# Kernel tuning notes

Hardware: AMD Instinct MI355X
Metric: run time of the kernel (lower is better)

The kernel has to match this reference:

```python
import jax, jax.numpy as jnp
import numpy as np
from math import ceil

H, W = 360, 640
H_, W_ = ceil(H / 32) * 32, ceil(W / 32) * 32  # 384, 640
SF = 2
TIMES = [k / SF for k in range(1, SF)]  # [0.5]


def conv(x, w, b=None, pad=1):
    y = jax.lax.conv_general_dilated(x, w, (1, 1), [(pad, pad), (pad, pad)],
                                     dimension_numbers=('NCHW', 'OIHW', 'NCHW'))
    if b is not None:
        y = y + b[None, :, None, None]
    return y


def resize_ac(x, Hn, Wn):
    # bilinear, align_corners=True, NCHW
    B, C, Hs, Ws = x.shape
    if (Hn, Wn) == (Hs, Ws):
        return x
    ys = jnp.linspace(0.0, Hs - 1.0, Hn, dtype=x.dtype)
    xs = jnp.linspace(0.0, Ws - 1.0, Wn, dtype=x.dtype)
    y0 = jnp.floor(ys).astype(jnp.int32); y1 = jnp.minimum(y0 + 1, Hs - 1)
    x0 = jnp.floor(xs).astype(jnp.int32); x1 = jnp.minimum(x0 + 1, Ws - 1)
    wy = (ys - y0)[None, None, :, None]
    wx = (xs - x0)[None, None, None, :]
    rows = x[:, :, y0, :] * (1 - wy) + x[:, :, y1, :] * wy      # [B,C,Hn,Ws]
    return rows[:, :, :, x0] * (1 - wx) + rows[:, :, :, x1] * wx  # [B,C,Hn,Wn]


def warp(img, flow):
    # backward warp with bilinear sampling, zeros padding (grid_sample semantics)
    B, C, Hs, Ws = img.shape
    gy, gx = jnp.meshgrid(jnp.arange(Hs, dtype=img.dtype), jnp.arange(Ws, dtype=img.dtype), indexing='ij')
    xq = gx[None] + flow[:, 0]  # [B,H,W]
    yq = gy[None] + flow[:, 1]

    def samp(im, xx, yy):  # im [C,H,W]
        x0 = jnp.floor(xx).astype(jnp.int32); x1 = x0 + 1
        y0 = jnp.floor(yy).astype(jnp.int32); y1 = y0 + 1
        wx = xx - x0; wy = yy - y0

        def g(xi, yi):
            valid = ((xi >= 0) & (xi < Ws) & (yi >= 0) & (yi < Hs)).astype(im.dtype)
            xc = jnp.clip(xi, 0, Ws - 1); yc = jnp.clip(yi, 0, Hs - 1)
            return im[:, yc, xc] * valid[None]  # [C,H,W] gather

        return (g(x0, y0) * (1 - wx) * (1 - wy) + g(x1, y0) * wx * (1 - wy)
                + g(x0, y1) * (1 - wx) * wy + g(x1, y1) * wx * wy)

    return jax.vmap(samp)(img, xq, yq)


def bmnet(x6, t, w1, b1, w2, b2):
    # stand-in bilateral motion net: conv stack conditioned on time channel -> 2-ch flow
    tch = jnp.full_like(x6[:, :1], t)
    h = jax.nn.relu(conv(jnp.concatenate([x6, tch], 1), w1, b1, 1))
    return conv(h, w2, b2, 1)


def local_expand(x):
    # [B,C,H,W] -> [B,C*9,H,W] of 3x3 neighborhoods (c-major, kernel-position minor)
    B, C, Hs, Ws = x.shape
    xp = jnp.pad(x, ((0, 0), (0, 0), (1, 1), (1, 1)))
    pats = [xp[:, :, dy:dy + Hs, dx:dx + Ws] for dy in range(3) for dx in range(3)]
    return jnp.stack(pats, 2).reshape(B, C * 9, Hs, Ws)


def dynfilter(cand, DF):
    # cand [B,6,H,W], DF [B,54,H,W] -> [B,1,H,W] spatially-varying weighted gather
    pe = local_expand(cand)
    return jnp.einsum('bkhw,bkhw->bhw', pe, DF)[:, None]


def reference(I0, I1, target, ctx_W, bm_W1, bm_b1, bm_W2, bm_b2, df_W1, df_b1, df_W2, df_b2, count):
    tgt = target.at[count].set(I0[0])
    c = count + 1
    pair_r = resize_ac(jnp.concatenate([I0, I1], 1), H_, W_)
    scl = jnp.array([W / W_, H / H_], jnp.float32).reshape(1, 2, 1, 1)
    F01 = resize_ac(bmnet(pair_r, 0.0, bm_W1, bm_b1, bm_W2, bm_b2) * 2.0, H, W) * scl
    F10 = resize_ac(bmnet(pair_r, 1.0, bm_W1, bm_b1, bm_W2, bm_b2) * -2.0, H, W) * scl
    CI0 = jax.nn.relu(conv(I0, ctx_W, None, 3))
    CI1 = jax.nn.relu(conv(I1, ctx_W, None, 3))
    X0 = jnp.concatenate([I0, CI0], 1)  # [1,67,H,W]
    X1 = jnp.concatenate([I1, CI1], 1)
    for t in TIMES:
        ti = 1.0 - t
        BM = resize_ac(bmnet(pair_r, t, bm_W1, bm_b1, bm_W2, bm_b2), H, W) * scl
        C1 = warp(X0, -t * F01)
        C2 = warp(X1, ti * F01)
        C3 = warp(X0, t * F10)
        C4 = warp(X1, (t - 1.0) * F10)
        C5 = warp(X0, BM * (-2.0 * t))
        C6 = warp(X1, BM * (2.0 * ti))
        inp = jnp.concatenate([I0, C1, C2, C3, C4, C5, C6, I1], 1)  # [1,408,H,W]
        h = jax.nn.relu(conv(inp, df_W1, df_b1, 1))
        DF = jax.nn.softmax(conv(h, df_W2, df_b2, 1), axis=1)  # [1,54,H,W]
        cand = inp[:, 3:-3]  # [1,402,H,W]
        R = dynfilter(cand[:, 0::67], DF)
        G = dynfilter(cand[:, 1::67], DF)
        Bc = dynfilter(cand[:, 2::67], DF)
        tgt = tgt.at[c, 0].set(R[0, 0]).at[c, 1].set(G[0, 0]).at[c, 2].set(Bc[0, 0])
        c += 1
    return tgt, c


def setup_inputs() -> dict:
    key = jax.random.key(0)
    ks = jax.random.split(key, 8)
    he = lambda k, shp: jax.random.normal(k, shp, jnp.float32) * np.float32((2.0 / (shp[1] * shp[2] * shp[3])) ** 0.5)
    return {
        'I0': jax.random.uniform(ks[0], (1, 3, H, W), jnp.float32),
        'I1': jax.random.uniform(ks[1], (1, 3, H, W), jnp.float32),
        'target': jnp.zeros((3, 3, H, W), jnp.float32),
        'ctx_W': he(ks[2], (64, 3, 7, 7)),
        'bm_W1': he(ks[3], (32, 7, 3, 3)),
        'bm_b1': jnp.zeros((32,), jnp.float32),
        'bm_W2': he(ks[4], (2, 32, 3, 3)) * np.float32(0.1),  # small flows
        'bm_b2': jnp.zeros((2,), jnp.float32),
        'df_W1': he(ks[5], (32, 408, 3, 3)),
        'df_b1': jnp.zeros((32,), jnp.float32),
        'df_W2': he(ks[6], (54, 32, 3, 3)),
        'df_b2': jnp.zeros((54,), jnp.float32),
        'count': 0,
    }
```

## Files before the change

kernel.cpp:

```cpp
#include <hip/hip_runtime.h>
#include <hip/hip_bf16.h>
#include <hip/hip_fp16.h>

#define Hh 360
#define Ww 640
#define HW (Hh*Ww)
#define Hr 384
#define HWr (Hr*Ww)

#define TW 48
#define TH 4
#define WCOLS 50
#define SROWS 6
#define NXT 14
#define NYT 90
#define NBLK (NXT*NYT)

#define WTW 16
#define WTH 8
#define WCL 18
#define WSR 10
#define WCCH 72
#define WNXT 40
#define WNYT 45
#define WNBLK (WNXT*WNYT)

#define CRS 24

typedef __hip_bfloat16 bf16;
typedef __attribute__((ext_vector_type(8))) short short8v;
typedef __attribute__((ext_vector_type(4))) short short4v;
typedef __attribute__((ext_vector_type(4))) float f32x4;
typedef __attribute__((ext_vector_type(2))) float f32x2;
typedef __attribute__((ext_vector_type(4))) int i32x4;

static __device__ __forceinline__ bf16 f2b(float v) { return __float2bfloat16(v); }
static __device__ __forceinline__ short f2bs(float v) { bf16 t = __float2bfloat16(v); return *(short*)&t; }
static __device__ __forceinline__ float bs2f(short s) {
    unsigned u = ((unsigned)(unsigned short)s) << 16;
    float f; __builtin_memcpy(&f, &u, 4); return f;
}

#if defined(__has_builtin)
#if __has_builtin(__builtin_amdgcn_cvt_pk_f32_fp8) && __has_builtin(__builtin_amdgcn_cvt_pk_fp8_f32)
#define FP8_HW 1
#endif
#endif

static __device__ __forceinline__ void fp8dec4(int dw, float* f) {
#ifdef FP8_HW
    f32x2 lo = __builtin_amdgcn_cvt_pk_f32_fp8(dw, false);
    f32x2 hi = __builtin_amdgcn_cvt_pk_f32_fp8(dw, true);
    f[0] = lo[0]; f[1] = lo[1]; f[2] = hi[0]; f[3] = hi[1];
#else
    #pragma unroll
    for (int k = 0; k < 4; k++) {
        int u = (dw >> (8 * k)) & 0xFF;
        int e = (u >> 3) & 15, m = u & 7;
        int mant = e ? ((8 + m) << (e - 1)) : m;
        float v = (float)mant * 0x1p-9f;
        f[k] = (u & 0x80) ? -v : v;
    }
#endif
}

static __device__ __forceinline__ int fp8enc4(float a, float b, float c, float d) {
#ifdef FP8_HW
    int r = __builtin_amdgcn_cvt_pk_fp8_f32(a, b, 0, false);
    r = __builtin_amdgcn_cvt_pk_fp8_f32(c, d, r, true);
    return r;
#else
    float vals[4] = {a, b, c, d};
    int r = 0;
    #pragma unroll
    for (int k = 0; k < 4; k++) {
        float v = vals[k];
        unsigned bits; __builtin_memcpy(&bits, &v, 4);
        unsigned s = bits >> 31;
        float av = fabsf(v);
        int u;
        if (!(av >= 0x1p-10f)) u = 0;
        else if (av >= 448.0f) u = 0x7E;
        else {
            int e; float fr = frexpf(av, &e);
            (void)fr;
            int E = e + 6;
            if (E < 1) {
                u = (int)roundf(av * 512.0f);
            } else {
                float sc = exp2f((float)(10 - E));
                int mm = (int)roundf(av * sc) - 8;
                if (mm == 8) { mm = 0; E++; }
                u = (E > 15) ? 0x7E : ((E << 3) | mm);
            }
        }
        r |= ((u | (s << 7)) & 0xFF) << (8 * k);
    }
    return r;
#endif
}

__global__ void front_all(const float* __restrict__ I0, const float* __restrict__ I1,
                          const float* __restrict__ target, const int* __restrict__ count,
                          const float* __restrict__ dfW1, const float* __restrict__ dfW2,
                          const float* __restrict__ ctxW, const float* __restrict__ bmW2,
                          const float* __restrict__ bmW1,
                          float* __restrict__ out, bf16* __restrict__ I4,
                          bf16* __restrict__ pr8,
                          bf16* __restrict__ wfrag, bf16* __restrict__ wfrag2,
                          bf16* __restrict__ wctx, float* __restrict__ w2t,
                          bf16* __restrict__ wbm1, float* __restrict__ tsW) {
    int idx = blockIdx.x * 256 + threadIdx.x;
    if (idx < 6 * HW + 1) {
        if (idx < 3 * HW) {
            out[idx] = I0[idx];
        } else if (idx < 6 * HW) {
            size_t off = (size_t)6 * HW + (idx - 3 * HW);
            out[off] = target[off];
        } else {
            out[(size_t)9 * HW] = (float)(count[0] + 2);
        }
        return;
    }
    idx -= 6 * HW + 1;
    if (idx < 2 * HW) {
        int z = idx / HW, p = idx % HW;
        const float* img = z ? I1 : I0;
        short4v v;
        v[0] = f2bs(img[p]);
        v[1] = f2bs(img[(size_t)HW + p]);
        v[2] = f2bs(img[(size_t)2 * HW + p]);
        v[3] = 0;
        *(short4v*)((short*)I4 + (size_t)idx * 4) = v;
        return;
    }
    idx -= 2 * HW;
    if (idx < HWr) {
        int p = idx;
        int x = p % Ww, y = p / Ww;
        float ys = y * (359.0f / 383.0f);
        int y0 = (int)floorf(ys);
        if (y0 > 359) y0 = 359;
        int y1 = y0 + 1; if (y1 > 359) y1 = 359;
        float wy = ys - (float)y0;
        short8v v;
        #pragma unroll
        for (int c = 0; c < 6; c++) {
            const float* src = (c < 3) ? (I0 + (size_t)c * HW) : (I1 + (size_t)(c - 3) * HW);
            v[c] = f2bs(src[y0 * Ww + x] * (1.0f - wy) + src[y1 * Ww + x] * wy);
        }
        v[6] = 0; v[7] = 0;
        *(short8v*)((short*)pr8 + (size_t)p * 8) = v;
        return;
    }
    idx -= HWr;
    if (idx < 165888) {
        int j = idx & 7;
        int t = idx >> 3;
        int l = t & 63; t >>= 6;
        int m = t & 1; t >>= 1;
        int chunk = t % 3; t /= 3;
        int q = t % 9;
        int w = t / 9;
        int oc = m * 16 + (l & 15);
        int ch = chunk * 32 + ((l >> 4) << 3) + j;
        int ic = -1;
        if (ch < 67) ic = 3 + 67 * w + ch;
        else if (ch < 70) {
            if (w == 0) ic = ch - 67;
            else if (w == 5) ic = 405 + (ch - 67);
        }
        float v = (ic >= 0) ? dfW1[((oc * 408 + ic) * 3 + q / 3) * 3 + (q % 3)] : 0.0f;
        wfrag[idx] = f2b(v);
        return;
    }
    idx -= 165888;
    if (idx < 18432) {
        int j = idx & 7;
        int t = idx >> 3;
        int l = t & 63; t >>= 6;
        int n = t & 3; t >>= 2;
        int q = t;
        int oc = n * 16 + (l & 15);
        int kch = ((l >> 4) << 3) + j;
        float v = (oc < 54) ? dfW2[((oc * 32 + kch) * 3 + q / 3) * 3 + (q % 3)] : 0.0f;
        wfrag2[idx] = f2b(v);
        return;
    }
    idx -= 18432;
    if (idx < 14336) {
        int j = idx & 7;
        int t = idx >> 3;
        int l = t & 63; t >>= 6;
        int n = t & 3;
        int ky = t >> 2;
        int oc = n * 16 + (l & 15);
        int k = ((l >> 4) << 3) + j;
        int kx = k >> 2, ic = k & 3;
        float v = (kx < 7 && ic < 3) ? ctxW[oc * 147 + ic * 49 + ky * 7 + kx] : 0.0f;
        wctx[idx] = f2b(v);
        return;
    }
    idx -= 14336;
    if (idx < 576) {
        int o = idx & 1;
        int t = idx >> 1;
        int i = t % 32;
        int q = t / 32;
        w2t[idx] = bmW2[o * 288 + i * 9 + q];
        return;
    }
    idx -= 576;
    if (idx < 3072) {
        int j = idx & 7;
        int t = idx >> 3;
        int l = t & 63; t >>= 6;
        int m = t & 1;
        int ky = t >> 1;
        int oc = m * 16 + (l & 15);
        int k = ((l >> 4) << 3) + j;
        int kx = k >> 3, ic = k & 7;
        float v = (kx < 3 && ic < 6) ? bmW1[oc * 63 + ic * 9 + ky * 3 + kx] : 0.0f;
        wbm1[idx] = f2b(v);
        return;
    }
    idx -= 3072;
    if (idx < 288) {
        int o = idx & 31;
        int c = idx >> 5;
        int vy = c / 3, vx = c % 3;
        float s = 0.0f;
        for (int q = 0; q < 9; q++) {
            int ky = q / 3, kx = q % 3;
            bool okY = !((vy == 1 && ky == 0) || (vy == 2 && ky == 2));
            bool okX = !((vx == 1 && kx == 0) || (vx == 2 && kx == 2));
            if (okY && okX) s += bmW1[o * 63 + 54 + q];
        }
        tsW[idx] = s;
    }
}

__global__ __launch_bounds__(256, 4) void bm_base_mfma(const bf16* __restrict__ pr8,
                                                       const bf16* __restrict__ wbm1,
                                                       const float* __restrict__ b1,
                                                       const float* __restrict__ tsW,
                                                       bf16* __restrict__ h) {
    __shared__ short raw8[SROWS * WCOLS * 8];
    __shared__ short outb[192 * 32];
    __shared__ float tsl[288];
    const int tid = threadIdx.x;
    const int bx = blockIdx.x % NXT;
    const int by = blockIdx.x / NXT;
    const int x0 = bx * TW, y0 = by * TH;
    const short8v z8 = {0, 0, 0, 0, 0, 0, 0, 0};

    for (int e = tid; e < 288; e += 256) tsl[e] = tsW[e];
    for (int e = tid; e < SROWS * WCOLS; e += 256) {
        int c = e % WCOLS, r = e / WCOLS;
        int gy = y0 - 1 + r, gx = x0 - 1 + c;
        short8v v = z8;
        if (gy >= 0 && gy < Hr && gx >= 0 && gx < Ww)
            v = *(const short8v*)((const short*)pr8 + ((size_t)gy * Ww + gx) * 8);
        *(short8v*)(raw8 + e * 8) = v;
    }
    __syncthreads();

    const int wv = tid >> 6, lane = tid & 63, l15 = lane & 15, lg = lane >> 4;
    f32x4 acc[3][2];
    {
        float bv0 = b1[l15], bv1 = b1[16 + l15];
        #pragma unroll
        for (int pt = 0; pt < 3; pt++)
            #pragma unroll
            for (int r = 0; r < 4; r++) { acc[pt][0][r] = bv0; acc[pt][1][r] = bv1; }
    }
    #pragma unroll 1
    for (int ky = 0; ky < 3; ky++) {
        short8v bw0 = ((const short8v*)wbm1)[(ky * 2 + 0) * 64 + lane];
        short8v bw1 = ((const short8v*)wbm1)[(ky * 2 + 1) * 64 + lane];
        #pragma unroll
        for (int pt = 0; pt < 3; pt++) {
            int col = pt * 16 + l15;
            short8v a = z8;
            if (lg < 3) a = *(const short8v*)(raw8 + ((wv + ky) * WCOLS + col + lg) * 8);
            acc[pt][0] = __builtin_amdgcn_mfma_f32_16x16x32_bf16(a, bw0, acc[pt][0], 0, 0, 0);
            acc[pt][1] = __builtin_amdgcn_mfma_f32_16x16x32_bf16(a, bw1, acc[pt][1], 0, 0, 0);
        }
    }
    #pragma unroll
    for (int pt = 0; pt < 3; pt++)
        #pragma unroll
        for (int m = 0; m < 2; m++)
            #pragma unroll
            for (int r = 0; r < 4; r++) {
                int px = pt * 16 + (lg << 2) + r;
                outb[(wv * 48 + px) * 32 + m * 16 + l15] = f2bs(acc[pt][m][r]);
            }
    __syncthreads();
    #pragma unroll
    for (int it = 0; it < 3; it++) {
        int e = it * 256 + tid;
        int oc8 = e & 3;
        int px = (e >> 2) % 48;
        int rw = e / 192;
        int gx = x0 + px;
        if (gx < Ww) {
            int gy = y0 + rw;
            short8v bsev = *(const short8v*)(outb + (rw * 48 + px) * 32 + oc8 * 8);
            int vy = (gy == 0) ? 1 : ((gy == Hr - 1) ? 2 : 0);
            int vx = (gx == 0) ? 1 : ((gx == Ww - 1) ? 2 : 0);
            const float* tp = tsl + (vy * 3 + vx) * 32 + oc8 * 8;
            float bsef[8], tsf[8];
            #pragma unroll
            for (int j = 0; j < 8; j++) { bsef[j] = bs2f(bsev[j]); tsf[j] = tp[j]; }
            #pragma unroll
            for (int z = 0; z < 3; z++) {
                float tz = (z == 0) ? 0.0f : ((z == 1) ? 1.0f : 0.5f);
                short8v o;
                #pragma unroll
                for (int j = 0; j < 8; j++)
                    o[j] = f2bs(fmaxf(bsef[j] + tz * tsf[j], 0.0f));
                *(short8v*)((short*)h + ((size_t)z * HWr + (size_t)gy * Ww + gx) * 32 + oc8 * 8) = o;
            }
        }
    }
}

__global__ __launch_bounds__(256) void bm_conv2i(const bf16* __restrict__ h,
                                                 const float* __restrict__ w2t,
                                                 const float* __restrict__ b2,
                                                 float* __restrict__ bmout) {
    int p = blockIdx.x * 256 + threadIdx.x;
    if (p >= HWr) return;
    int z = blockIdx.y;
    int x = p % Ww, y = p / Ww;
    const short* hz = (const short*)h + (size_t)z * HWr * 32;
    float a0 = b2[0], a1 = b2[1];
    for (int ky = 0; ky < 3; ky++) {
        int ny = y + ky - 1;
        if (ny < 0 || ny >= Hr) continue;
        for (int kx = 0; kx < 3; kx++) {
            int nx = x + kx - 1;
            if (nx < 0 || nx >= Ww) continue;
            const float* wp = w2t + (ky * 3 + kx) * 64;
            const short* ip = hz + ((size_t)ny * Ww + nx) * 32;
            #pragma unroll
            for (int ck = 0; ck < 4; ck++) {
                short8v v = *(const short8v*)(ip + ck * 8);
                #pragma unroll
                for (int j = 0; j < 8; j++) {
                    float f = bs2f(v[j]);
                    a0 = fmaf(f, wp[(ck * 8 + j) * 2 + 0], a0);
                    a1 = fmaf(f, wp[(ck * 8 + j) * 2 + 1], a1);
                }
            }
        }
    }
    float f = (z == 0) ? 2.0f : ((z == 1) ? -2.0f : 1.0f);
    bmout[(size_t)(z * 2 + 0) * HWr + p] = a0 * f;
    bmout[(size_t)(z * 2 + 1) * HWr + p] = a1 * f;
}

__global__ __launch_bounds__(256) void flow_resize(const float* __restrict__ bmout,
                                                   float* __restrict__ flows) {
    int p = blockIdx.x * 256 + threadIdx.x;
    if (p >= HW) return;
    int x = p % Ww;
    int y = p / Ww;
    float ys = y * (383.0f / 359.0f);
    int y0 = (int)floorf(ys);
    if (y0 > 383) y0 = 383;
    int y1 = y0 + 1; if (y1 > 383) y1 = 383;
    float wy = ys - (float)y0;
    float o[6];
    #pragma unroll
    for (int zc = 0; zc < 6; zc++) {
        const float* src = bmout + (size_t)zc * HWr;
        float v = src[y0 * Ww + x] * (1.0f - wy) + src[y1 * Ww + x] * wy;
        o[zc] = v * ((zc & 1) ? (360.0f / 384.0f) : 1.0f);
    }
    #pragma unroll
    for (int zc = 0; zc < 6; zc++)
        flows[(size_t)p * 6 + zc] = o[zc];
}

__global__ __launch_bounds__(256, 2) void ctx_mfma(const bf16* __restrict__ I4,
                                                   const bf16* __restrict__ wctx,
                                                   bf16* __restrict__ Xrgb,
                                                   unsigned char* __restrict__ Xq) {
    __shared__ short raw4[10 * 54 * 4];
    __shared__ short outb[192 * 72];
    const int tid = threadIdx.x;
    const int z = blockIdx.y;
    const int bx = blockIdx.x % NXT;
    const int by = blockIdx.x / NXT;
    const int x0 = bx * TW, y0 = by * TH;
    const short* img4 = (const short*)I4 + (size_t)z * HW * 4;
    const short4v z4 = {0, 0, 0, 0};

    for (int e = tid; e < 540; e += 256) {
        int c = e % 54, r = e / 54;
        int gy = y0 - 3 + r, gx = x0 - 3 + c;
        short4v v = z4;
        if (gy >= 0 && gy < Hh && gx >= 0 && gx < Ww)
            v = *(const short4v*)(img4 + ((size_t)gy * Ww + gx) * 4);
        *(short4v*)(raw4 + e * 4) = v;
    }
    __syncthreads();

    const int wv = tid >> 6, lane = tid & 63, l15 = lane & 15, lg = lane >> 4;
    f32x4 acc[3][4];
    #pragma unroll
    for (int pt = 0; pt < 3; pt++)
        #pragma unroll
        for (int n = 0; n < 4; n++)
            #pragma unroll
            for (int r = 0; r < 4; r++) acc[pt][n][r] = 0.0f;

    #pragma unroll 1
    for (int ky = 0; ky < 7; ky++) {
        short8v bw[4];
        #pragma unroll
        for (int n = 0; n < 4; n++)
            bw[n] = ((const short8v*)wctx)[(ky * 4 + n) * 64 + lane];
        #pragma unroll
        for (int pt = 0; pt < 3; pt++) {
            int col = pt * 16 + l15;
            int base = ((wv + ky) * 54 + col + 2 * lg) * 4;
            short4v lo = *(const short4v*)(raw4 + base);
            short4v hi = (lg == 3) ? z4 : *(const short4v*)(raw4 + base + 4);
            short8v a = __builtin_shufflevector(lo, hi, 0, 1, 2, 3, 4, 5, 6, 7);
            #pragma unroll
            for (int n = 0; n < 4; n++)
                acc[pt][n] = __builtin_amdgcn_mfma_f32_16x16x32_bf16(a, bw[n], acc[pt][n], 0, 0, 0);
        }
    }

    for (int e = tid; e < 576; e += 256) {
        int ic = e % 3, p = e / 3;
        outb[p * 72 + ic] = raw4[((p / 48 + 3) * 54 + (p % 48) + 3) * 4 + ic];
    }
    for (int e = tid; e < 960; e += 256) {
        int c = e % 5, p = e / 5;
        outb[p * 72 + 67 + c] = 0;
    }
    #pragma unroll
    for (int pt = 0; pt < 3; pt++)
        #pragma unroll
        for (int n = 0; n < 4; n++)
            #pragma unroll
            for (int r = 0; r < 4; r++) {
                int px = pt * 16 + (lg << 2) + r;
                outb[(wv * 48 + px) * 72 + 3 + n * 16 + l15] = f2bs(fmaxf(acc[pt][n][r], 0.0f));
            }
    __syncthreads();
    for (int e = tid; e < 960; e += 256) {
        int part = e % 5, p = e / 5;
        int gx = x0 + p % 48, gy = y0 + p / 48;
        if (gx >= Ww) continue;
        size_t pix = (size_t)z * HW + (size_t)gy * Ww + gx;
        if (part == 0) {
            *(short8v*)((short*)Xrgb + pix * 8) = *(const short8v*)(outb + p * 72);
        } else {
            const short* src = outb + p * 72 + 8 + (part - 1) * 16;
            i32x4 r;
            #pragma unroll
            for (int d = 0; d < 4; d++)
                r[d] = fp8enc4(bs2f(src[4 * d + 0]), bs2f(src[4 * d + 1]),
                               bs2f(src[4 * d + 2]), bs2f(src[4 * d + 3]));
            *(i32x4*)(Xq + pix * 64 + (size_t)(part - 1) * 16) = r;
        }
    }
}

__global__ __launch_bounds__(256, 3) void wdf_all(const bf16* __restrict__ Xrgb,
                                                  const unsigned char* __restrict__ Xq,
                                                  const float* __restrict__ flows,
                                                  const bf16* __restrict__ wfrag,
                                                  const float* __restrict__ b1,
                                                  const float* __restrict__ I0,
                                                  const float* __restrict__ I1,
                                                  bf16* __restrict__ hdf,
                                                  bf16* __restrict__ candRGB) {
    __shared__ short ldsA[WSR * WCL * WCCH];
    __shared__ short ldsB[WSR * WCL * WCCH];
    const int tid = threadIdx.x;
    const int bid = blockIdx.x;
    const int wg = (bid & 7) * (WNBLK / 8) + (bid >> 3);
    const int bx = wg % WNXT;
    const int by = wg / WNXT;
    const int x0 = bx * WTW, y0 = by * WTH;
    const short8v z8 = {0, 0, 0, 0, 0, 0, 0, 0};

    const int wv = tid >> 6;
    const int lane = tid & 63;
    const int l15 = lane & 15;
    const int lg = lane >> 4;

    auto stage = [&](int w, short* dstb) {
        const int fz = (w < 2) ? 0 : ((w < 4) ? 1 : 2);
        const float fac = ((w < 4) ? 0.5f : 1.0f) *
                          ((w == 1 || w == 2 || w == 5) ? 1.0f : -1.0f);
        const short* xrgb = (const short*)Xrgb + (size_t)(w & 1) * HW * 8;
        const unsigned char* xq = Xq + (size_t)(w & 1) * HW * 64;
        const float* img = (w == 0) ? I0 : I1;
        int e = tid;
        if (e < WSR * WCL) {
            int c = e % WCL, r = e / WCL;
            int gy = y0 - 1 + r, gx = x0 - 1 + c;
            short* dst = dstb + e * WCCH;
            if (gy < 0 || gy >= Hh || gx < 0 || gx >= Ww) {
                #pragma unroll
                for (int ck = 0; ck < 9; ck++) *(short8v*)(dst + ck * 8) = z8;
            } else {
                int p = gy * Ww + gx;
                float2 fl = *(const float2*)(flows + (size_t)p * 6 + fz * 2);
                float xqf = (float)gx + fl.x * fac;
                float yqf = (float)gy + fl.y * fac;
                float fx0 = floorf(xqf), fy0 = floorf(yqf);
                int sx0 = (int)fx0, sy0 = (int)fy0;
                int sx1 = sx0 + 1, sy1 = sy0 + 1;
                float wx = xqf - fx0, wy = yqf - fy0;
                float vx0 = (sx0 >= 0 && sx0 < Ww) ? 1.0f : 0.0f;
                float vx1 = (sx1 >= 0 && sx1 < Ww) ? 1.0f : 0.0f;
                float vy0 = (sy0 >= 0 && sy0 < Hh) ? 1.0f : 0.0f;
                float vy1 = (sy1 >= 0 && sy1 < Hh) ? 1.0f : 0.0f;
                int cx0 = min(max(sx0, 0), Ww - 1), cx1 = min(max(sx1, 0), Ww - 1);
                int cy0 = min(max(sy0, 0), Hh - 1), cy1 = min(max(sy1, 0), Hh - 1);
                float w00 = (1.0f - wx) * (1.0f - wy) * vx0 * vy0;
                float w10 = wx * (1.0f - wy) * vx1 * vy0;
                float w01 = (1.0f - wx) * wy * vx0 * vy1;
                float w11 = wx * wy * vx1 * vy1;
                size_t i00 = (size_t)cy0 * Ww + cx0;
                size_t i10 = (size_t)cy0 * Ww + cx1;
                size_t i01 = (size_t)cy1 * Ww + cx0;
                size_t i11 = (size_t)cy1 * Ww + cx1;
                short8v g00 = *(const short8v*)(xrgb + i00 * 8);
                short8v g10 = *(const short8v*)(xrgb + i10 * 8);
                short8v g01 = *(const short8v*)(xrgb + i01 * 8);
                short8v g11 = *(const short8v*)(xrgb + i11 * 8);
                const i32x4* q00 = (const i32x4*)(xq + i00 * 64);
                const i32x4* q10 = (const i32x4*)(xq + i10 * 64);
                const i32x4* q01 = (const i32x4*)(xq + i01 * 64);
                const i32x4* q11 = (const i32x4*)(xq + i11 * 64);
                i32x4 qa[4], qb[4], qc[4], qd[4];
                #pragma unroll
                for (int c2 = 0; c2 < 4; c2++) {
                    qa[c2] = q00[c2]; qb[c2] = q10[c2];
                    qc[c2] = q01[c2]; qd[c2] = q11[c2];
                }
                short rgb0, rgb1, rgb2;
                {
                    short8v o;
                    #pragma unroll
                    for (int j = 0; j < 8; j++) {
                        float v = w00 * bs2f(g00[j]) + w10 * bs2f(g10[j]) +
                                  w01 * bs2f(g01[j]) + w11 * bs2f(g11[j]);
                        o[j] = f2bs(v);
                    }
                    rgb0 = o[0]; rgb1 = o[1]; rgb2 = o[2];
                    *(short8v*)(dst) = o;
                }
                #pragma unroll
                for (int c2 = 0; c2 < 4; c2++) {
                    short o16[16];
                    #pragma unroll
                    for (int d = 0; d < 4; d++) {
                        float fa[4], fb[4], fc[4], fd[4];
                        fp8dec4(qa[c2][d], fa);
                        fp8dec4(qb[c2][d], fb);
                        fp8dec4(qc[c2][d], fc);
                        fp8dec4(qd[c2][d], fd);
                        #pragma unroll
                        for (int j = 0; j < 4; j++) {
                            float v = w00 * fa[j] + w10 * fb[j] +
                                      w01 * fc[j] + w11 * fd[j];
                            o16[4 * d + j] = f2bs(v);
                        }
                    }
                    short8v o1, o2;
                    #pragma unroll
                    for (int j = 0; j < 8; j++) { o1[j] = o16[j]; o2[j] = o16[8 + j]; }
                    *(short8v*)(dst + 8 + c2 * 16) = o1;
                    *(short8v*)(dst + 8 + c2 * 16 + 8) = o2;
                }
                if (w == 0 || w == 5) {
                    dst[67] = f2bs(img[p]);
                    dst[68] = f2bs(img[(size_t)HW + p]);
                    dst[69] = f2bs(img[(size_t)2 * HW + p]);
                }
                if (r >= 1 && r <= WTH && c >= 1 && c <= WTW) {
                    short* crp = (short*)candRGB + (size_t)p * CRS + w * 3;
                    crp[0] = rgb0; crp[1] = rgb1; crp[2] = rgb2;
                }
            }
        }
    };

    f32x4 acc[2][2];
    {
        float bv0 = b1[l15], bv1 = b1[16 + l15];
        #pragma unroll
        for (int rt = 0; rt < 2; rt++)
            #pragma unroll
            for (int r = 0; r < 4; r++) { acc[rt][0][r] = bv0; acc[rt][1][r] = bv1; }
    }

    stage(0, ldsA);
    __syncthreads();

    #pragma unroll 1
    for (int wi = 0; wi < 6; wi++) {
        const int w = (wi < 3) ? (2 * wi) : (2 * (wi - 3) + 1);
        short* curb = (wi & 1) ? ldsB : ldsA;

        const short8v* wf = (const short8v*)(wfrag + (size_t)w * 9 * 3 * 2 * 64 * 8);
        __builtin_amdgcn_s_setprio(1);
        #pragma unroll 1
        for (int ky = 0; ky < 3; ky++) {
            #pragma unroll
            for (int kx = 0; kx < 3; kx++) {
                const int dx = kx - 1;
                const int q = ky * 3 + kx;
                #pragma unroll
                for (int chunk = 0; chunk < 3; chunk++) {
                    short8v bw0 = wf[((q * 3 + chunk) * 2 + 0) * 64 + lane];
                    short8v bw1 = wf[((q * 3 + chunk) * 2 + 1) * 64 + lane];
                    const int koff = (chunk < 2) ? (chunk * 32 + (lg << 3)) : 64;
                    #pragma unroll
                    for (int rt = 0; rt < 2; rt++) {
                        int srow = 2 * wv + rt + ky;
                        int col = 1 + dx + l15;
                        const short8v* apt = (const short8v*)(curb + (srow * WCL + col) * WCCH + koff);
                        short8v a = *apt;
                        acc[rt][0] = __builtin_amdgcn_mfma_f32_16x16x32_bf16(a, bw0, acc[rt][0], 0, 0, 0);
                        acc[rt][1] = __builtin_amdgcn_mfma_f32_16x16x32_bf16(a, bw1, acc[rt][1], 0, 0, 0);
                    }
                }
            }
        }
        __builtin_amdgcn_s_setprio(0);

        if (wi < 5) {
            const int wn = ((wi + 1) < 3) ? (2 * (wi + 1)) : (2 * (wi + 1 - 3) + 1);
            stage(wn, (wi & 1) ? ldsA : ldsB);
        }
        __syncthreads();
    }

    #pragma unroll
    for (int rt = 0; rt < 2; rt++) {
        #pragma unroll
        for (int m = 0; m < 2; m++) {
            #pragma unroll
            for (int r = 0; r < 4; r++) {
                float v = fmaxf(acc[rt][m][r], 0.0f);
                int pxx = (lg << 2) + r;
                ldsA[((2 * wv + rt) * 16 + pxx) * 32 + m * 16 + l15] = f2bs(v);
            }
        }
    }
    __syncthreads();
    #pragma unroll
    for (int it = 0; it < 2; it++) {
        int e = it * 256 + tid;
        int oc8 = e & 3;
        int px = e >> 2;
        int row = px >> 4, xl = px & 15;
        short8v v = *(const short8v*)(ldsA + px * 32 + oc8 * 8);
        *(short8v*)((short*)hdf + ((size_t)(y0 + row) * Ww + x0 + xl) * 32 + oc8 * 8) = v;
    }
}

__global__ __launch_bounds__(256, 3) void df2_mfma(const bf16* __restrict__ hdf,
                                                   const bf16* __restrict__ wf2,
                                                   const float* __restrict__ b2,
                                                   const bf16* __restrict__ candRGB,
                                                   float* __restrict__ out) {
    __shared__ float smem[192 * 65];
    short* sst = (short*)smem;
    const int tid = threadIdx.x;
    const int bx = blockIdx.x % NXT;
    const int by = blockIdx.x / NXT;
    const int x0 = bx * TW, y0 = by * TH;

    const short* hs = (const short*)hdf;
    for (int e = tid; e < SROWS * WCOLS * 4; e += 256) {
        int v = e & 3;
        int c = (e >> 2) % WCOLS;
        int r = e / (4 * WCOLS);
        int gy = y0 - 1 + r, gx = x0 - 1 + c;
        short8v val = {0, 0, 0, 0, 0, 0, 0, 0};
        if (gy >= 0 && gy < Hh && gx >= 0 && gx < Ww)
            val = *(const short8v*)(hs + ((size_t)gy * Ww + gx) * 32 + v * 8);
        *(short8v*)(sst + (r * WCOLS + c) * 32 + v * 8) = val;
    }
    __syncthreads();

    const int wv = tid >> 6, lane = tid & 63, l15 = lane & 15, lg = lane >> 4;
    f32x4 acc[3][4];
    #pragma unroll
    for (int n = 0; n < 4; n++) {
        int oc = n * 16 + l15;
        float bv = (oc < 54) ? b2[oc] : 0.0f;
        #pragma unroll
        for (int pt = 0; pt < 3; pt++)
            #pragma unroll
            for (int r = 0; r < 4; r++) acc[pt][n][r] = bv;
    }
    #pragma unroll 1
    for (int ky = 0; ky < 3; ky++) {
        int srow = wv + ky;
        #pragma unroll
        for (int kx = 0; kx < 3; kx++) {
            int dx = kx - 1, q = ky * 3 + kx;
            short8v bw[4];
            #pragma unroll
            for (int n = 0; n < 4; n++) bw[n] = ((const short8v*)wf2)[(q * 4 + n) * 64 + lane];
            #pragma unroll
            for (int pt = 0; pt < 3; pt++) {
                int col = 1 + pt * 16 + dx + l15;
                short8v a = *(const short8v*)(sst + (srow * WCOLS + col) * 32 + lg * 8);
                #pragma unroll
                for (int n = 0; n < 4; n++)
                    acc[pt][n] = __builtin_amdgcn_mfma_f32_16x16x32_bf16(a, bw[n], acc[pt][n], 0, 0, 0);
            }
        }
    }
    __syncthreads();
    #pragma unroll
    for (int pt = 0; pt < 3; pt++)
        #pragma unroll
        for (int n = 0; n < 4; n++)
            #pragma unroll
            for (int r = 0; r < 4; r++) {
                int px = wv * 48 + pt * 16 + (lg << 2) + r;
                smem[px * 65 + n * 16 + l15] = acc[pt][n][r];
            }
    __syncthreads();

    if (tid < 192) {
        int xl = tid % 48, yl = tid / 48;
        int gx = x0 + xl, gy = y0 + yl;
        if (gx < Ww) {
            const float* lp = smem + tid * 65;
            float m = lp[0];
            #pragma unroll
            for (int o = 1; o < 54; o++) m = fmaxf(m, lp[o]);
            float e[54]; float s = 0.f;
            #pragma unroll
            for (int o = 0; o < 54; o++) { e[o] = __expf(lp[o] - m); s += e[o]; }
            float inv = 1.0f / s;
            float rr = 0, gg = 0, bb = 0;
            const short* cr = (const short*)candRGB;
            #pragma unroll
            for (int dy = 0; dy < 3; dy++) {
                int ny = gy + dy - 1;
                if (ny < 0 || ny >= Hh) continue;
                #pragma unroll
                for (int dx = 0; dx < 3; dx++) {
                    int nx = gx + dx - 1;
                    if (nx < 0 || nx >= Ww) continue;
                    const short* cp = cr + ((size_t)ny * Ww + nx) * CRS;
                    short8v v0 = *(const short8v*)(cp);
                    short8v v1 = *(const short8v*)(cp + 8);
                    short8v v2 = *(const short8v*)(cp + 16);
                    float ch[18];
                    #pragma unroll
                    for (int j = 0; j < 8; j++) { ch[j] = bs2f(v0[j]); ch[8 + j] = bs2f(v1[j]); }
                    ch[16] = bs2f(v2[0]);
                    ch[17] = bs2f(v2[1]);
                    #pragma unroll
                    for (int c6 = 0; c6 < 6; c6++) {
                        float df = e[c6 * 9 + dy * 3 + dx];
                        rr = fmaf(ch[c6 * 3 + 0], df, rr);
                        gg = fmaf(ch[c6 * 3 + 1], df, gg);
                        bb = fmaf(ch[c6 * 3 + 2], df, bb);
                    }
                }
            }
            size_t gp = (size_t)gy * Ww + gx;
            out[(size_t)3 * HW + gp] = rr * inv;
            out[(size_t)4 * HW + gp] = gg * inv;
            out[(size_t)5 * HW + gp] = bb * inv;
        }
    }
}

static inline int cdiv(int a, int b) { return (a + b - 1) / b; }

extern "C" void kernel_launch(void* const* d_in, const int* in_sizes, int n_in,
                              void* d_out, int out_size, void* d_ws, size_t ws_size,
                              hipStream_t stream) {
    const float* I0 = (const float*)d_in[0];
    const float* I1 = (const float*)d_in[1];
    const float* target = (const float*)d_in[2];
    const float* ctx_W = (const float*)d_in[3];
    const float* bm_W1 = (const float*)d_in[4];
    const float* bm_b1 = (const float*)d_in[5];
    const float* bm_W2 = (const float*)d_in[6];
    const float* bm_b2 = (const float*)d_in[7];
    const float* df_W1 = (const float*)d_in[8];
    const float* df_b1 = (const float*)d_in[9];
    const float* df_W2 = (const float*)d_in[10];
    const float* df_b2 = (const float*)d_in[11];
    const int* count = (const int*)d_in[12];
    float* out = (float*)d_out;

    char* ws = (char*)d_ws;
    size_t off = 0;
    auto alloc = [&](size_t bytes) -> char* {
        char* p = ws + off;
        off += (bytes + 255) & ~(size_t)255;
        return p;
    };
    char* xreg = alloc((size_t)3 * HWr * 32 * 2);
    float* flows = (float*)alloc((size_t)HW * 6 * 4);
    bf16* candRGB = (bf16*)alloc((size_t)HW * CRS * 2);
    bf16* hdf = (bf16*)alloc((size_t)HW * 32 * 2);
    bf16* I4 = (bf16*)alloc((size_t)2 * HW * 4 * 2);
    bf16* pr8 = (bf16*)alloc((size_t)HWr * 8 * 2);
    float* bmout = (float*)alloc((size_t)6 * HWr * 4);
    bf16* wfrag = (bf16*)alloc((size_t)165888 * 2);
    bf16* wfrag2 = (bf16*)alloc((size_t)18432 * 2);
    bf16* wctx = (bf16*)alloc((size_t)14336 * 2);
    float* w2t = (float*)alloc((size_t)576 * 4);
    bf16* wbm1 = (bf16*)alloc((size_t)3072 * 2);
    float* tsW = (float*)alloc((size_t)288 * 4);
    size_t need = off;
    if (ws_size < need) return;

    bf16* h_bm = (bf16*)xreg;
    bf16* Xrgb = (bf16*)xreg;
    unsigned char* Xq = (unsigned char*)(xreg + (size_t)2 * HW * 8 * 2);

    const int FRONT_TOTAL = (6 * HW + 1) + 2 * HW + HWr + 202592;
    front_all<<<cdiv(FRONT_TOTAL, 256), 256, 0, stream>>>(
        I0, I1, target, count, df_W1, df_W2, ctx_W, bm_W2, bm_W1,
        out, I4, pr8, wfrag, wfrag2, wctx, w2t, wbm1, tsW);

    bm_base_mfma<<<NXT * (Hr / TH), 256, 0, stream>>>(pr8, wbm1, bm_b1, tsW, h_bm);
    dim3 g1(cdiv(HWr, 256), 3);
    bm_conv2i<<<g1, 256, 0, stream>>>(h_bm, w2t, bm_b2, bmout);
    flow_resize<<<cdiv(HW, 256), 256, 0, stream>>>(bmout, flows);

    dim3 gc(NBLK, 2);
    ctx_mfma<<<gc, 256, 0, stream>>>(I4, wctx, Xrgb, Xq);

    wdf_all<<<WNBLK, 256, 0, stream>>>(Xrgb, Xq, flows, wfrag, df_b1, I0, I1, hdf, candRGB);

    df2_mfma<<<NBLK, 256, 0, stream>>>(hdf, wfrag2, df_b2, candRGB, out);
}
```

Baseline: 252.7 us.

## Rewrite bm conv2 as LDS-tiled bf16 MFMA kernel with padded weight fragments

Replaces the scalar per-pixel 32->2 channel 3x3 convolution with an MFMA kernel that stages a halo tile of the hidden activations in shared memory. Each wave then computes 16-pixel strips using 16x16x32 bf16 MFMA, with the output channels zero-padded from 2 to 16. The weight prep in the front kernel now emits bf16 MFMA fragments instead of transposed fp32 weights. The aim is to cut redundant global loads and scalar FMAs, at the cost of wasted MFMA lanes on padded channels. Separately, ctx_mfma's launch bound is raised to 4 blocks per CU, which may increase register pressure.

Result: faster. 242.8 us (-3.9%).

```diff
diff --git a/kernel.cpp b/kernel.cpp
--- a/kernel.cpp
+++ b/kernel.cpp
@@ -108,7 +108,7 @@
                           float* __restrict__ out, bf16* __restrict__ I4,
                           bf16* __restrict__ pr8,
                           bf16* __restrict__ wfrag, bf16* __restrict__ wfrag2,
-                          bf16* __restrict__ wctx, float* __restrict__ w2t,
+                          bf16* __restrict__ wctx, bf16* __restrict__ wbm2,
                           bf16* __restrict__ wbm1, float* __restrict__ tsW) {
     int idx = blockIdx.x * 256 + threadIdx.x;
     if (idx < 6 * HW + 1) {
@@ -202,15 +202,18 @@
         return;
     }
     idx -= 14336;
-    if (idx < 576) {
-        int o = idx & 1;
-        int t = idx >> 1;
-        int i = t % 32;
-        int q = t / 32;
-        w2t[idx] = bmW2[o * 288 + i * 9 + q];
+    if (idx < 4608) {
+        int j = idx & 7;
+        int t = idx >> 3;
+        int l = t & 63;
+        int q = t >> 6;
+        int oc = l & 15;
+        int kch = ((l >> 4) << 3) + j;
+        float v = (oc < 2) ? bmW2[oc * 288 + kch * 9 + q] : 0.0f;
+        wbm2[idx] = f2b(v);
         return;
     }
-    idx -= 576;
+    idx -= 4608;
     if (idx < 3072) {
         int j = idx & 7;
         int t = idx >> 3;
@@ -326,39 +329,67 @@
     }
 }
 
-__global__ __launch_bounds__(256) void bm_conv2i(const bf16* __restrict__ h,
-                                                 const float* __restrict__ w2t,
-                                                 const float* __restrict__ b2,
-                                                 float* __restrict__ bmout) {
-    int p = blockIdx.x * 256 + threadIdx.x;
-    if (p >= HWr) return;
-    int z = blockIdx.y;
-    int x = p % Ww, y = p / Ww;
+__global__ __launch_bounds__(256, 4) void bm2_mfma(const bf16* __restrict__ h,
+                                                   const bf16* __restrict__ wbm2,
+                                                   const float* __restrict__ b2,
+                                                   float* __restrict__ bmout) {
+    __shared__ short sst[SROWS * WCOLS * 32];
+    const int tid = threadIdx.x;
+    const int z = blockIdx.y;
+    const int bx = blockIdx.x % NXT;
+    const int by = blockIdx.x / NXT;
+    const int x0 = bx * TW, y0 = by * TH;
+    const short8v z8 = {0, 0, 0, 0, 0, 0, 0, 0};
+
     const short* hz = (const short*)h + (size_t)z * HWr * 32;
-    float a0 = b2[0], a1 = b2[1];
+    for (int e = tid; e < SROWS * WCOLS * 4; e += 256) {
+        int v = e & 3;
+        int c = (e >> 2) % WCOLS;
+        int r = e / (4 * WCOLS);
+        int gy = y0 - 1 + r, gx = x0 - 1 + c;
+        short8v val = z8;
+        if (gy >= 0 && gy < Hr && gx >= 0 && gx < Ww)
+            val = *(const short8v*)(hz + ((size_t)gy * Ww + gx) * 32 + v * 8);
+        *(short8v*)(sst + (r * WCOLS + c) * 32 + v * 8) = val;
+    }
+    __syncthreads();
+
+    const int wv = tid >> 6, lane = tid & 63, l15 = lane & 15, lg = lane >> 4;
+    f32x4 acc[3];
+    {
+        float bv = (l15 < 2) ? b2[l15] : 0.0f;
+        #pragma unroll
+        for (int pt = 0; pt < 3; pt++)
+            #pragma unroll
+            for (int r = 0; r < 4; r++) acc[pt][r] = bv;
+    }
+    #pragma unroll 1
     for (int ky = 0; ky < 3; ky++) {
-        int ny = y + ky - 1;
-        if (ny < 0 || ny >= Hr) continue;
+        int srow = wv + ky;
+        #pragma unroll
         for (int kx = 0; kx < 3; kx++) {
-            int nx = x + kx - 1;
-            if (nx < 0 || nx >= Ww) continue;
-            const float* wp = w2t + (ky * 3 + kx) * 64;
-            const short* ip = hz + ((size_t)ny * Ww + nx) * 32;
-            #pragma unroll
-            for (int ck = 0; ck < 4; ck++) {
-                short8v v = *(const short8v*)(ip + ck * 8);
-                #pragma unroll
-                for (int j = 0; j < 8; j++) {
-                    float f = bs2f(v[j]);
-                    a0 = fmaf(f, wp[(ck * 8 + j) * 2 + 0], a0);
-                    a1 = fmaf(f, wp[(ck * 8 + j) * 2 + 1], a1);
-                }
-            }
-        }
-    }
-    float f = (z == 0) ? 2.0f : ((z == 1) ? -2.0f : 1.0f);
-    bmout[(size_t)(z * 2 + 0) * HWr + p] = a0 * f;
-    bmout[(size_t)(z * 2 + 1) * HWr + p] = a1 * f;
+            int dx = kx - 1, q = ky * 3 + kx;
+            short8v bw = ((const short8v*)wbm2)[q * 64 + lane];
+            #pragma unroll
+            for (int pt = 0; pt < 3; pt++) {
+                int col = 1 + pt * 16 + dx + l15;
+                short8v a = *(const short8v*)(sst + (srow * WCOLS + col) * 32 + lg * 8);
+                acc[pt] = __builtin_amdgcn_mfma_f32_16x16x32_bf16(a, bw, acc[pt], 0, 0, 0);
+            }
+        }
+    }
+    const float f = (z == 0) ? 2.0f : ((z == 1) ? -2.0f : 1.0f);
+    if (l15 < 2) {
+        int gy = y0 + wv;
+        #pragma unroll
+        for (int pt = 0; pt < 3; pt++)
+            #pragma unroll
+            for (int r = 0; r < 4; r++) {
+                int gx = x0 + pt * 16 + (lg << 2) + r;
+                if (gx < Ww)
+                    bmout[(size_t)(z * 2 + l15) * HWr + (size_t)gy * Ww + gx] = acc[pt][r] * f;
+            }
+    }
 }
 
 __global__ __launch_bounds__(256) void flow_resize(const float* __restrict__ bmout,
@@ -384,7 +415,7 @@
         flows[(size_t)p * 6 + zc] = o[zc];
 }
 
-__global__ __launch_bounds__(256, 2) void ctx_mfma(const bf16* __restrict__ I4,
+__global__ __launch_bounds__(256, 4) void ctx_mfma(const bf16* __restrict__ I4,
                                                    const bf16* __restrict__ wctx,
                                                    bf16* __restrict__ Xrgb,
                                                    unsigned char* __restrict__ Xq) {
@@ -824,7 +855,7 @@
     bf16* wfrag = (bf16*)alloc((size_t)165888 * 2);
     bf16* wfrag2 = (bf16*)alloc((size_t)18432 * 2);
     bf16* wctx = (bf16*)alloc((size_t)14336 * 2);
-    float* w2t = (float*)alloc((size_t)576 * 4);
+    bf16* wbm2 = (bf16*)alloc((size_t)4608 * 2);
     bf16* wbm1 = (bf16*)alloc((size_t)3072 * 2);
     float* tsW = (float*)alloc((size_t)288 * 4);
     size_t need = off;
@@ -834,14 +865,14 @@
     bf16* Xrgb = (bf16*)xreg;
     unsigned char* Xq = (unsigned char*)(xreg + (size_t)2 * HW * 8 * 2);
 
-    const int FRONT_TOTAL = (6 * HW + 1) + 2 * HW + HWr + 202592;
+    const int FRONT_TOTAL = (6 * HW + 1) + 2 * HW + HWr + 206624;
     front_all<<<cdiv(FRONT_TOTAL, 256), 256, 0, stream>>>(
         I0, I1, target, count, df_W1, df_W2, ctx_W, bm_W2, bm_W1,
-        out, I4, pr8, wfrag, wfrag2, wctx, w2t, wbm1, tsW);
+        out, I4, pr8, wfrag, wfrag2, wctx, wbm2, wbm1, tsW);
 
     bm_base_mfma<<<NXT * (Hr / TH), 256, 0, stream>>>(pr8, wbm1, bm_b1, tsW, h_bm);
-    dim3 g1(cdiv(HWr, 256), 3);
-    bm_conv2i<<<g1, 256, 0, stream>>>(h_bm, w2t, bm_b2, bmout);
+    dim3 g2(NXT * (Hr / TH), 3);
+    bm2_mfma<<<g2, 256, 0, stream>>>(h_bm, wbm2, bm_b2, bmout);
     flow_resize<<<cdiv(HW, 256), 256, 0, stream>>>(bmout, flows);
 
     dim3 gc(NBLK, 2);
```
